# Optimization experiments

Measured on AMD Instinct MI355X. Metric: run time of the kernel, lower is better.

The kernel has to match this reference:

```python
import jax, jax.numpy as jnp
import numpy as np
from math import factorial

# ---- static configuration (matches init_kwargs) ----
IRREPS_IN1 = [(32, 0, 1), (32, 1, -1), (32, 2, 1)]   # (mul, l, parity)
IRREPS_SH  = [(1, 0, 1), (1, 1, -1), (1, 2, 1)]
IRREPS_OUT = [(32, 0, 1), (32, 1, -1), (32, 2, 1)]
NUM_BASIS = 10
HIDDEN = 16
CUTOFF = 4.0
P_ENV = 6  # dimenet envelope_exponent (5) + 1

# ---- real Wigner 3j (Clebsch-Gordan in real SH basis), computed once in numpy ----
def _su2_cg(j1, j2, j3, m1, m2, m3):
    if m3 != m1 + m2:
        return 0.0
    f = factorial
    vmin = max(-j1 + j2 + m3, -j1 + m1, 0)
    vmax = min(j2 + j3 + m1, j3 - j1 + j2, j3 + m3)
    c = (f(2*j3+1) * f(j3+j1-j2) * f(j3-j1+j2) * f(j1+j2-j3) / f(j1+j2+j3+1)
         * f(j3+m3) * f(j3-m3) / (f(j1+m1) * f(j1-m1) * f(j2+m2) * f(j2-m2))) ** 0.5
    s = 0.0
    for v in range(vmin, vmax + 1):
        s += (-1)**(v + j2 + m2) * f(j2+j3+m1-v) * f(j1-m1+v) / (
             f(v) * f(j3-j1+j2-v) * f(j3+m3-v) * f(v+j1-j2-m3))
    return c * s

def _q(l):  # real -> complex SH change of basis
    q = np.zeros((2*l+1, 2*l+1), dtype=complex)
    for m in range(-l, 0):
        q[l+m, l+abs(m)] = 2**-0.5
        q[l+m, l-abs(m)] = -1j * 2**-0.5
    q[l, l] = 1.0
    for m in range(1, l+1):
        q[l+m, l+abs(m)] = (-1)**m * 2**-0.5
        q[l+m, l-abs(m)] = 1j * (-1)**m * 2**-0.5
    return (-1j)**l * q

def _wigner_3j(l1, l2, l3):
    csu2 = np.array([[[ _su2_cg(l1, l2, l3, m1, m2, m3)
                       for m3 in range(-l3, l3+1)]
                      for m2 in range(-l2, l2+1)]
                     for m1 in range(-l1, l1+1)], dtype=complex)
    c = np.einsum('ij,kl,mn,ikm->jln', _q(l1), _q(l2), np.conj(_q(l3)), csu2)
    c = np.real(c)
    n = np.linalg.norm(c)
    return c / n if n > 0 else c

def _slices(irreps):
    s, off = [], 0
    for mul, l, p in irreps:
        d = mul * (2*l + 1)
        s.append((off, off + d))
        off += d
    return s, off

SL1, DIM_IN1 = _slices(IRREPS_IN1)
SL2, DIM_SH = _slices(IRREPS_SH)
SL3, DIM_OUT = _slices(IRREPS_OUT)

_raw = []
for i1, (m1, l1, p1) in enumerate(IRREPS_IN1):
    for i2, (m2, l2, p2) in enumerate(IRREPS_SH):
        for i3, (m3, l3, p3) in enumerate(IRREPS_OUT):
            if p1 * p2 == p3 and abs(l1 - l2) <= l3 <= l1 + l2:
                _raw.append((i1, i2, i3))

_fan = {}
for i1, i2, i3 in _raw:  # path_normalization='element': fan-in per output slot
    _fan[i3] = _fan.get(i3, 0) + IRREPS_IN1[i1][0] * IRREPS_SH[i2][0]

INSTR = []
WEIGHT_NUMEL = 0
for i1, i2, i3 in _raw:
    m1, l1, _ = IRREPS_IN1[i1]
    m2, l2, _ = IRREPS_SH[i2]
    m3, l3, _ = IRREPS_OUT[i3]
    pw = ((2*l3 + 1) / _fan[i3]) ** 0.5  # irrep_normalization='component'
    C = _wigner_3j(l1, l2, l3).astype(np.float32)
    INSTR.append((i1, i2, i3, m1, l1, m2, l2, m3, l3, WEIGHT_NUMEL, pw, C))
    WEIGHT_NUMEL += m1 * m2 * m3

# ---- radial network: Bessel basis (with dimenet envelope) -> Linear -> SiLU -> Linear ----
def _radial(distance, freq, W1, b1, W2, b2):
    d = distance[:, 0]                      # squeeze(-1) -> [E]
    x = (d / CUTOFF)[:, None]               # [E, 1]
    p = P_ENV
    a = -(p + 1) * (p + 2) / 2.0
    b = float(p * (p + 2))
    c = -p * (p + 1) / 2.0
    env = (1.0 / x + a * x**(p-1) + b * x**p + c * x**(p+1)) * (x < 1.0).astype(x.dtype)
    basis = env * jnp.sin(freq * x)         # [E, NUM_BASIS]
    h = jax.nn.silu(basis @ W1 + b1)
    return h @ W2 + b2                      # [E, WEIGHT_NUMEL]

# ---- fully connected tensor product (uvw, external per-edge weights) ----
def _tp(x, sh, weights):
    E = x.shape[0]
    acc = [jnp.zeros((E, m, 2*l + 1), x.dtype) for m, l, _ in IRREPS_OUT]
    for (i1, i2, i3, m1, l1, m2, l2, m3, l3, woff, pw, C) in INSTR:
        a, b = SL1[i1]; xb = x[:, a:b].reshape(E, m1, 2*l1 + 1)
        a, b = SL2[i2]; sb = sh[:, a:b].reshape(E, m2, 2*l2 + 1)
        w = weights[:, woff:woff + m1*m2*m3].reshape(E, m1, m2, m3)
        Cj = jnp.asarray(C)
        acc[i3] = acc[i3] + pw * jnp.einsum('euvw,ijk,eui,evj->ewk', w, Cj, xb, sb)
    return jnp.concatenate([a.reshape(E, -1) for a in acc], axis=1)


def setup_inputs() -> dict:
    key = jax.random.key(0)
    ks = jax.random.split(key, 6)
    E = 16384
    x = jax.random.normal(ks[0], (E, DIM_IN1), jnp.float32)
    rel_pos_sh = jax.random.normal(ks[1], (E, DIM_SH), jnp.float32)
    # distances strictly inside (0, cutoff) so envelope 1/x and mask are benign
    distance = 0.25 + 3.5 * jax.random.uniform(ks[2], (E, 1), jnp.float32)
    freq = jnp.pi * jnp.arange(1, NUM_BASIS + 1, dtype=jnp.float32)
    W1 = 0.4 * jax.random.normal(ks[3], (NUM_BASIS, HIDDEN), jnp.float32)
    b1 = jnp.zeros((HIDDEN,), jnp.float32)
    W2 = 0.1 * jax.random.normal(ks[4], (HIDDEN, WEIGHT_NUMEL), jnp.float32)
    b2 = jnp.zeros((WEIGHT_NUMEL,), jnp.float32)
    return {"x": x, "rel_pos_sh": rel_pos_sh, "distance": distance,
            "freq": freq, "W1": W1, "b1": b1, "W2": W2, "b2": b2}


def reference(x, rel_pos_sh, distance, freq, W1, b1, W2, b2):
    weights = _radial(distance, freq, W1, b1, W2, b2)
    return _tp(x, rel_pos_sh, weights)
```

## Files before the change

kernel.cpp:

```cpp
#include <hip/hip_runtime.h>
#include <cmath>
#include <complex>
#include <cstring>
#include <algorithm>

#define DIM_IN  288
#define DIM_SHD 9
#define NB      10
#define NH      16
#define EPB     16
#define BLOCK   256
#define NINSTR  11
#define XSTR    292
#define ZW_STRIDE 44
#define ZW_SIZE   704
#define W2B_ELEMS (NINSTR * 32 * 32 * 32)

#define OFF_XO 0
#define OFF_ZW 4672
#define OFF_SH 7488
#define POOLSZ 7680

typedef __attribute__((ext_vector_type(8))) short  short8b;
typedef __attribute__((ext_vector_type(4))) float  f32x4;
typedef __attribute__((ext_vector_type(2))) float  f32x2;

__device__ float g_C[NINSTR][125];

__device__ __forceinline__ unsigned short f2bf(float f) {
  unsigned int u = __float_as_uint(f);
  unsigned int r = (u + 0x7fffu + ((u >> 16) & 1u)) >> 16;
  return (unsigned short)r;
}

__global__ __launch_bounds__(256) void prep_w2(const float* __restrict__ W2,
                                               const float* __restrict__ b2,
                                               unsigned short* __restrict__ W2b) {
  int gid = blockIdx.x * 256 + threadIdx.x;
  if (gid < W2B_ELEMS) {
    int c = gid >> 5, t = gid & 31;
    float v = (t < 16) ? W2[(size_t)t * 11264 + c] : (t == 16 ? b2[c] : 0.0f);
    W2b[gid] = f2bf(v);
  }
}

template<int INS,int D1,int D2,int D3,int OFF1,int OFF2>
__device__ __forceinline__ void z_phase_q(
    int lane, int q, const float* __restrict__ s_x,
    const float* __restrict__ s_sh, float* __restrict__ zw)
{
  const float* __restrict__ Cp = g_C[INS];
  constexpr int NP = D3 / 2;
  #pragma unroll
  for (int s = 0; s < 2; ++s) {
    int id = lane + s * 64;
    int e = id >> 3, ul = id & 7;
    const float* xe = s_x + e * XSTR + OFF1 + (q * 8 + ul) * D1;
    f32x2 zk2[NP > 0 ? NP : 1];
    float zkl = 0.f;
    #pragma unroll
    for (int m = 0; m < NP; ++m) zk2[m] = (f32x2){0.f, 0.f};
    #pragma unroll
    for (int i = 0; i < D1; ++i) {
      float xv = xe[i];
      #pragma unroll
      for (int j = 0; j < D2; ++j) {
        float pr = xv * s_sh[e * 12 + OFF2 + j];
        f32x2 pr2 = {pr, pr};
        const float* cb = Cp + (i * D2 + j) * D3;
        #pragma unroll
        for (int m = 0; m < NP; ++m) {
          f32x2 cc = {cb[2 * m], cb[2 * m + 1]};
          zk2[m] = __builtin_elementwise_fma(cc, pr2, zk2[m]);
        }
        zkl = fmaf(cb[D3 - 1], pr, zkl);
      }
    }
    float* zo = zw + e * ZW_STRIDE + ul;
    #pragma unroll
    for (int m = 0; m < NP; ++m) {
      zo[(2 * m) * 8]     = zk2[m].x;
      zo[(2 * m + 1) * 8] = zk2[m].y;
    }
    zo[(D3 - 1) * 8] = zkl;
  }
}

template<int INS,int D3,int SB>
__device__ __forceinline__ void contract_q(
    int ls, int lq, int q,
    const unsigned short* __restrict__ W2b,
    const float* __restrict__ zw, short8b hB, f32x2 (&acc)[2][2][9])
{
  const unsigned short* Ap =
      W2b + ((size_t)(INS * 32 + q * 8) * 32 + ls) * 32 + lq * 8;
  const float* zb = zw + ls * ZW_STRIDE;
  const f32x4 zero4 = {0.f, 0.f, 0.f, 0.f};

  short8b R0c = *(const short8b*)(Ap);
  short8b R1c = *(const short8b*)(Ap + 512);
  short8b R0n = *(const short8b*)(Ap + 1024);
  short8b R1n = *(const short8b*)(Ap + 1536);
  f32x4 w0_cur = __builtin_amdgcn_mfma_f32_16x16x32_bf16(R0c, hB, zero4, 0, 0, 0);
  f32x4 w1_cur = __builtin_amdgcn_mfma_f32_16x16x32_bf16(R1c, hB, zero4, 0, 0, 0);

  #pragma unroll
  for (int c = 0; c < 2; ++c) {
    float4 zq[D3];
    #pragma unroll
    for (int k = 0; k < D3; ++k)
      zq[k] = *(const float4*)(zb + k * 8 + c * 4);
    #pragma unroll
    for (int i = 0; i < 4; ++i) {
      const int g = c * 4 + i;
      f32x4 w0n, w1n;
      if (g < 7) {
        w0n = __builtin_amdgcn_mfma_f32_16x16x32_bf16(R0n, hB, zero4, 0, 0, 0);
        w1n = __builtin_amdgcn_mfma_f32_16x16x32_bf16(R1n, hB, zero4, 0, 0, 0);
        if (g + 2 < 8) {
          R0n = *(const short8b*)(Ap + (size_t)(g + 2) * 1024);
          R1n = *(const short8b*)(Ap + (size_t)(g + 2) * 1024 + 512);
        }
      }
      f32x2 w0lo = {w0_cur[0], w0_cur[1]};
      f32x2 w0hi = {w0_cur[2], w0_cur[3]};
      f32x2 w1lo = {w1_cur[0], w1_cur[1]};
      f32x2 w1hi = {w1_cur[2], w1_cur[3]};
      #pragma unroll
      for (int k = 0; k < D3; ++k) {
        const float zz = (i == 0) ? zq[k].x : (i == 1) ? zq[k].y
                       : (i == 2) ? zq[k].z : zq[k].w;
        f32x2 zv = {zz, zz};
        acc[0][0][SB + k] = __builtin_elementwise_fma(w0lo, zv, acc[0][0][SB + k]);
        acc[0][1][SB + k] = __builtin_elementwise_fma(w0hi, zv, acc[0][1][SB + k]);
        acc[1][0][SB + k] = __builtin_elementwise_fma(w1lo, zv, acc[1][0][SB + k]);
        acc[1][1][SB + k] = __builtin_elementwise_fma(w1hi, zv, acc[1][1][SB + k]);
      }
      if (g < 7) { w0_cur = w0n; w1_cur = w1n; }
    }
  }
}

__global__ __launch_bounds__(BLOCK, 2) void conv_kernel(
    const float* __restrict__ xg, const float* __restrict__ shg,
    const float* __restrict__ dist, const float* __restrict__ freq,
    const float* __restrict__ W1, const float* __restrict__ b1,
    const unsigned short* __restrict__ W2b,
    float* __restrict__ out)
{
  __shared__ float s_pool[POOLSZ];
  float* s_xo = s_pool + OFF_XO;
  float* s_sh = s_pool + OFF_SH;

  const int tid = threadIdx.x;
  const int e0 = blockIdx.x * EPB;
  const int lane = tid & 63;
  const int ls = lane & 15;
  const int lq = lane >> 4;
  const int q   = tid >> 6;
  float* zw = s_pool + OFF_ZW + q * ZW_SIZE;
  float* s_basis = s_pool + OFF_ZW + 2 * ZW_SIZE;
  unsigned short* s_hb = (unsigned short*)(s_pool + OFF_ZW + 3 * ZW_SIZE);

  for (int i4 = tid; i4 < EPB * 72; i4 += BLOCK) {
    int e = i4 / 72, r = i4 - e * 72;
    *(float4*)(s_xo + e * XSTR + r * 4) =
        *(const float4*)(xg + (size_t)(e0 + e) * DIM_IN + r * 4);
  }
  if (tid < EPB * DIM_SHD) {
    int e = tid / DIM_SHD, c = tid - (tid / DIM_SHD) * DIM_SHD;
    s_sh[e * 12 + c] = shg[(size_t)(e0 + e) * DIM_SHD + c];
  }
  if (tid < EPB * NB) {
    int e = tid / NB, n = tid - (tid / NB) * NB;
    float d  = dist[e0 + e];
    float xv = d * 0.25f;
    float x2 = xv * xv, x4 = x2 * x2, x5 = x4 * xv;
    float env = 1.0f / xv + x5 * fmaf(xv, fmaf(xv, -21.0f, 48.0f), -28.0f);
    env = (xv < 1.0f) ? env : 0.0f;
    s_basis[e * NB + n] = env * sinf(freq[n] * xv);
  }
  __syncthreads();

  {
    int e = tid >> 4, t = tid & 15;
    float v = b1[t];
    #pragma unroll
    for (int n = 0; n < NB; ++n) v = fmaf(s_basis[e * NB + n], W1[n * NH + t], v);
    v = v / (1.0f + expf(-v));
    s_hb[e * 32 + t] = f2bf(v);
    s_hb[e * 32 + t + 16] = (t == 0) ? (unsigned short)0x3F80 : (unsigned short)0;
  }
  __syncthreads();
  short8b hB = *(const short8b*)(s_hb + ls * 32 + lq * 8);
  __syncthreads();

  f32x2 acc[2][2][9];
  #pragma unroll
  for (int wt = 0; wt < 2; ++wt)
    #pragma unroll
    for (int p = 0; p < 2; ++p)
      #pragma unroll
      for (int a = 0; a < 9; ++a) acc[wt][p][a] = (f32x2){0.f, 0.f};

  z_phase_q< 0, 1, 1, 1,   0, 0>(lane, q, s_xo, s_sh, zw);
  contract_q< 0, 1, 0>(ls, lq, q, W2b, zw, hB, acc);
  z_phase_q< 1, 1, 3, 3,   0, 1>(lane, q, s_xo, s_sh, zw);
  contract_q< 1, 3, 1>(ls, lq, q, W2b, zw, hB, acc);
  z_phase_q< 2, 1, 5, 5,   0, 4>(lane, q, s_xo, s_sh, zw);
  contract_q< 2, 5, 4>(ls, lq, q, W2b, zw, hB, acc);
  z_phase_q< 3, 3, 1, 3,  32, 0>(lane, q, s_xo, s_sh, zw);
  contract_q< 3, 3, 1>(ls, lq, q, W2b, zw, hB, acc);
  z_phase_q< 4, 3, 3, 1,  32, 1>(lane, q, s_xo, s_sh, zw);
  contract_q< 4, 1, 0>(ls, lq, q, W2b, zw, hB, acc);
  z_phase_q< 5, 3, 3, 5,  32, 1>(lane, q, s_xo, s_sh, zw);
  contract_q< 5, 5, 4>(ls, lq, q, W2b, zw, hB, acc);
  z_phase_q< 6, 3, 5, 3,  32, 4>(lane, q, s_xo, s_sh, zw);
  contract_q< 6, 3, 1>(ls, lq, q, W2b, zw, hB, acc);
  z_phase_q< 7, 5, 1, 5, 128, 0>(lane, q, s_xo, s_sh, zw);
  contract_q< 7, 5, 4>(ls, lq, q, W2b, zw, hB, acc);
  z_phase_q< 8, 5, 3, 3, 128, 1>(lane, q, s_xo, s_sh, zw);
  contract_q< 8, 3, 1>(ls, lq, q, W2b, zw, hB, acc);
  z_phase_q< 9, 5, 5, 1, 128, 4>(lane, q, s_xo, s_sh, zw);
  contract_q< 9, 1, 0>(ls, lq, q, W2b, zw, hB, acc);
  z_phase_q<10, 5, 5, 5, 128, 4>(lane, q, s_xo, s_sh, zw);
  contract_q<10, 5, 4>(ls, lq, q, W2b, zw, hB, acc);

  __syncthreads();
  #pragma unroll
  for (int ph = 3; ph >= 0; --ph) {
    if (q == ph) {
      float* row = s_xo + ls * XSTR;
      #pragma unroll
      for (int wt = 0; wt < 2; ++wt) {
        #pragma unroll
        for (int r = 0; r < 4; ++r) {
          const int w = wt * 16 + lq * 4 + r;
          float vals[9];
          #pragma unroll
          for (int a = 0; a < 9; ++a)
            vals[a] = (r & 1) ? acc[wt][r >> 1][a].y : acc[wt][r >> 1][a].x;
          if (ph == 3) {
            row[w] = vals[0];
            #pragma unroll
            for (int k = 0; k < 3; ++k) row[32 + w * 3 + k] = vals[1 + k];
            #pragma unroll
            for (int k = 0; k < 5; ++k) row[128 + w * 5 + k] = vals[4 + k];
          } else {
            row[w] += vals[0];
            #pragma unroll
            for (int k = 0; k < 3; ++k) row[32 + w * 3 + k] += vals[1 + k];
            #pragma unroll
            for (int k = 0; k < 5; ++k) row[128 + w * 5 + k] += vals[4 + k];
          }
        }
      }
    }
    __syncthreads();
  }
  for (int i4 = tid; i4 < EPB * 72; i4 += BLOCK) {
    int e = i4 / 72, r = i4 - e * 72;
    float4 v = *(const float4*)(s_xo + e * XSTR + r * 4);
    *(float4*)(out + (size_t)(e0 + e) * DIM_IN + r * 4) = v;
  }
}

typedef std::complex<double> cd;

static double factd(int n) { double r = 1; for (int i = 2; i <= n; ++i) r *= i; return r; }

static double su2_cg(int j1, int j2, int j3, int m1, int m2, int m3) {
  if (m3 != m1 + m2) return 0.0;
  int vmin = std::max(std::max(-j1 + j2 + m3, -j1 + m1), 0);
  int vmax = std::min(std::min(j2 + j3 + m1, j3 - j1 + j2), j3 + m3);
  if (vmax < vmin) return 0.0;
  double c = std::sqrt(
      factd(2*j3+1) * factd(j3+j1-j2) * factd(j3-j1+j2) * factd(j1+j2-j3) / factd(j1+j2+j3+1)
      * factd(j3+m3) * factd(j3-m3)
      / (factd(j1+m1) * factd(j1-m1) * factd(j2+m2) * factd(j2-m2)));
  double s = 0.0;
  for (int v = vmin; v <= vmax; ++v) {
    double sg = ((v + j2 + m2) & 1) ? -1.0 : 1.0;
    s += sg * factd(j2+j3+m1-v) * factd(j1-m1+v)
         / (factd(v) * factd(j3-j1+j2-v) * factd(j3+m3-v) * factd(v+j1-j2-m3));
  }
  return c * s;
}

static void qmat(int l, cd q[5][5]) {
  for (int a = 0; a < 5; ++a) for (int b = 0; b < 5; ++b) q[a][b] = cd(0, 0);
  const double s = 1.0 / std::sqrt(2.0);
  for (int m = -l; m < 0; ++m) {
    q[l + m][l - m] = cd(s, 0);
    q[l + m][l + m] = cd(0, -s);
  }
  q[l][l] = cd(1, 0);
  for (int m = 1; m <= l; ++m) {
    double sg = (m & 1) ? -1.0 : 1.0;
    q[l + m][l + m] = cd(sg * s, 0);
    q[l + m][l - m] = cd(0, sg * s);
  }
  cd ph = (l == 0) ? cd(1, 0) : (l == 1) ? cd(0, -1) : cd(-1, 0);
  for (int a = 0; a < 5; ++a) for (int b = 0; b < 5; ++b) q[a][b] *= ph;
}

static void wigner3j(int l1, int l2, int l3, double C[5][5][5]) {
  int d1 = 2*l1+1, d2 = 2*l2+1, d3 = 2*l3+1;
  cd q1[5][5], q2[5][5], q3[5][5];
  qmat(l1, q1); qmat(l2, q2); qmat(l3, q3);
  double norm2 = 0;
  for (int j = 0; j < d1; ++j)
    for (int l = 0; l < d2; ++l)
      for (int n = 0; n < d3; ++n) {
        cd sum(0, 0);
        for (int i = 0; i < d1; ++i)
          for (int k = 0; k < d2; ++k)
            for (int m = 0; m < d3; ++m) {
              double cg = su2_cg(l1, l2, l3, i - l1, k - l2, m - l3);
              if (cg != 0.0) sum += q1[i][j] * q2[k][l] * std::conj(q3[m][n]) * cg;
            }
        C[j][l][n] = sum.real();
        norm2 += C[j][l][n] * C[j][l][n];
      }
  double nrm = std::sqrt(norm2);
  if (nrm > 0)
    for (int j = 0; j < d1; ++j)
      for (int l = 0; l < d2; ++l)
        for (int n = 0; n < d3; ++n) C[j][l][n] /= nrm;
}

static void build_C_host(float C_out[NINSTR][125]) {
  const int L1[NINSTR] = {0,0,0,1,1,1,1,2,2,2,2};
  const int L2[NINSTR] = {0,1,2,0,1,1,2,0,1,2,2};
  const int L3[NINSTR] = {0,1,2,1,0,2,1,2,1,0,2};
  std::memset(C_out, 0, sizeof(float) * NINSTR * 125);
  for (int ins = 0; ins < NINSTR; ++ins) {
    int l1 = L1[ins], l2 = L2[ins], l3 = L3[ins];
    int d1 = 2*l1+1, d2 = 2*l2+1, d3 = 2*l3+1;
    double C[5][5][5];
    wigner3j(l1, l2, l3, C);
    double fan = (l3 == 0) ? 96.0 : 128.0;
    double pw = std::sqrt((2*l3+1) / fan);
    for (int i = 0; i < d1; ++i)
      for (int j = 0; j < d2; ++j)
        for (int k = 0; k < d3; ++k)
          C_out[ins][(i * d2 + j) * d3 + k] = (float)(pw * C[i][j][k]);
  }
}

extern "C" void kernel_launch(void* const* d_in, const int* in_sizes, int n_in,
                              void* d_out, int out_size, void* d_ws, size_t ws_size,
                              hipStream_t stream) {
  static float hC[NINSTR][125];
  build_C_host(hC);
  void* dC = nullptr;
  hipGetSymbolAddress(&dC, HIP_SYMBOL(g_C));
  hipMemcpyAsync(dC, hC, sizeof(hC), hipMemcpyHostToDevice, stream);

  const float* xg   = (const float*)d_in[0];
  const float* shg  = (const float*)d_in[1];
  const float* dist = (const float*)d_in[2];
  const float* freq = (const float*)d_in[3];
  const float* W1   = (const float*)d_in[4];
  const float* b1   = (const float*)d_in[5];
  const float* W2   = (const float*)d_in[6];
  const float* b2   = (const float*)d_in[7];
  float* out = (float*)d_out;
  unsigned short* W2b = (unsigned short*)d_ws;

  prep_w2<<<(W2B_ELEMS + 255) / 256, 256, 0, stream>>>(W2, b2, W2b);

  int E = in_sizes[2];
  int blocks = E / EPB;
  conv_kernel<<<blocks, BLOCK, 0, stream>>>(xg, shg, dist, freq, W1, b1, W2b, out);
}
```

Before: 70.64 us.

## Group z-phase by input irrep, load x directly from global into registers

Each wave now loads its x slice straight from global memory into registers once per input irrep and computes all of that irrep's CG-contracted z values in one pass. The results go into a larger per-wave z buffer with slot offsets, and the matching contractions then run back to back. This drops the shared-memory staging of x and repeated x reloads per instruction, and frees LDS by reusing the pool for the output gather. The cost is uncoalesced strided global loads of x, more registers held live, and a larger per-wave z buffer.

Result: faster. 68.27 us, median of 5 (-3.4%).

```diff
diff --git a/kernel.cpp b/kernel.cpp
--- a/kernel.cpp
+++ b/kernel.cpp
@@ -12,14 +12,12 @@
 #define BLOCK   256
 #define NINSTR  11
 #define XSTR    292
-#define ZW_STRIDE 44
-#define ZW_SIZE   704
+#define ZG_STRIDE 116
+#define ZG_SIZE  (16 * ZG_STRIDE)
 #define W2B_ELEMS (NINSTR * 32 * 32 * 32)
 
-#define OFF_XO 0
-#define OFF_ZW 4672
-#define OFF_SH 7488
-#define POOLSZ 7680
+#define OFF_SH 7424
+#define POOLSZ 7616
 
 typedef __attribute__((ext_vector_type(8))) short  short8b;
 typedef __attribute__((ext_vector_type(4))) float  f32x4;
@@ -44,49 +42,102 @@
   }
 }
 
-template<int INS,int D1,int D2,int D3,int OFF1,int OFF2>
-__device__ __forceinline__ void z_phase_q(
-    int lane, int q, const float* __restrict__ s_x,
-    const float* __restrict__ s_sh, float* __restrict__ zw)
+template<int INS,int D1,int D2,int D3,int OFF2,int SLOT>
+__device__ __forceinline__ void z_one(const float (&xv)[D1],
+                                      const float* __restrict__ she,
+                                      float* __restrict__ zo)
 {
   const float* __restrict__ Cp = g_C[INS];
   constexpr int NP = D3 / 2;
+  f32x2 zk2[NP > 0 ? NP : 1];
+  float zkl = 0.f;
+  #pragma unroll
+  for (int m = 0; m < NP; ++m) zk2[m] = (f32x2){0.f, 0.f};
+  #pragma unroll
+  for (int i = 0; i < D1; ++i) {
+    #pragma unroll
+    for (int j = 0; j < D2; ++j) {
+      float pr = xv[i] * she[OFF2 + j];
+      f32x2 pr2 = {pr, pr};
+      const float* cb = Cp + (i * D2 + j) * D3;
+      #pragma unroll
+      for (int m = 0; m < NP; ++m) {
+        f32x2 cc = {cb[2 * m], cb[2 * m + 1]};
+        zk2[m] = __builtin_elementwise_fma(cc, pr2, zk2[m]);
+      }
+      zkl = fmaf(cb[D3 - 1], pr, zkl);
+    }
+  }
+  #pragma unroll
+  for (int m = 0; m < NP; ++m) {
+    zo[(SLOT + 2 * m) * 8]     = zk2[m].x;
+    zo[(SLOT + 2 * m + 1) * 8] = zk2[m].y;
+  }
+  zo[(SLOT + D3 - 1) * 8] = zkl;
+}
+
+template<int D1,int OFF1>
+__device__ __forceinline__ void load_x(const float* __restrict__ xg, int e0,
+                                       int e, int u, float (&xv)[D1]) {
+  const float* xp = xg + (size_t)(e0 + e) * DIM_IN + OFF1 + u * D1;
+  #pragma unroll
+  for (int i = 0; i < D1; ++i) xv[i] = xp[i];
+}
+
+__device__ __forceinline__ void z_group_l0(int lane, int q, int e0,
+    const float* __restrict__ xg, const float* __restrict__ s_sh,
+    float* __restrict__ zw) {
   #pragma unroll
   for (int s = 0; s < 2; ++s) {
     int id = lane + s * 64;
-    int e = id >> 3, ul = id & 7;
-    const float* xe = s_x + e * XSTR + OFF1 + (q * 8 + ul) * D1;
-    f32x2 zk2[NP > 0 ? NP : 1];
-    float zkl = 0.f;
-    #pragma unroll
-    for (int m = 0; m < NP; ++m) zk2[m] = (f32x2){0.f, 0.f};
-    #pragma unroll
-    for (int i = 0; i < D1; ++i) {
-      float xv = xe[i];
-      #pragma unroll
-      for (int j = 0; j < D2; ++j) {
-        float pr = xv * s_sh[e * 12 + OFF2 + j];
-        f32x2 pr2 = {pr, pr};
-        const float* cb = Cp + (i * D2 + j) * D3;
-        #pragma unroll
-        for (int m = 0; m < NP; ++m) {
-          f32x2 cc = {cb[2 * m], cb[2 * m + 1]};
-          zk2[m] = __builtin_elementwise_fma(cc, pr2, zk2[m]);
-        }
-        zkl = fmaf(cb[D3 - 1], pr, zkl);
-      }
-    }
-    float* zo = zw + e * ZW_STRIDE + ul;
-    #pragma unroll
-    for (int m = 0; m < NP; ++m) {
-      zo[(2 * m) * 8]     = zk2[m].x;
-      zo[(2 * m + 1) * 8] = zk2[m].y;
-    }
-    zo[(D3 - 1) * 8] = zkl;
-  }
-}
-
-template<int INS,int D3,int SB>
+    int e = id >> 3, ul = id & 7, u = q * 8 + ul;
+    float xv[1];
+    load_x<1, 0>(xg, e0, e, u, xv);
+    const float* she = s_sh + e * 12;
+    float* zo = zw + e * ZG_STRIDE + ul;
+    z_one<0, 1, 1, 1, 0, 0>(xv, she, zo);
+    z_one<1, 1, 3, 3, 1, 1>(xv, she, zo);
+    z_one<2, 1, 5, 5, 4, 4>(xv, she, zo);
+  }
+}
+
+__device__ __forceinline__ void z_group_l1(int lane, int q, int e0,
+    const float* __restrict__ xg, const float* __restrict__ s_sh,
+    float* __restrict__ zw) {
+  #pragma unroll
+  for (int s = 0; s < 2; ++s) {
+    int id = lane + s * 64;
+    int e = id >> 3, ul = id & 7, u = q * 8 + ul;
+    float xv[3];
+    load_x<3, 32>(xg, e0, e, u, xv);
+    const float* she = s_sh + e * 12;
+    float* zo = zw + e * ZG_STRIDE + ul;
+    z_one<3, 3, 1, 3, 0, 0>(xv, she, zo);
+    z_one<4, 3, 3, 1, 1, 3>(xv, she, zo);
+    z_one<5, 3, 3, 5, 1, 4>(xv, she, zo);
+    z_one<6, 3, 5, 3, 4, 9>(xv, she, zo);
+  }
+}
+
+__device__ __forceinline__ void z_group_l2(int lane, int q, int e0,
+    const float* __restrict__ xg, const float* __restrict__ s_sh,
+    float* __restrict__ zw) {
+  #pragma unroll
+  for (int s = 0; s < 2; ++s) {
+    int id = lane + s * 64;
+    int e = id >> 3, ul = id & 7, u = q * 8 + ul;
+    float xv[5];
+    load_x<5, 128>(xg, e0, e, u, xv);
+    const float* she = s_sh + e * 12;
+    float* zo = zw + e * ZG_STRIDE + ul;
+    z_one< 7, 5, 1, 5, 0, 0>(xv, she, zo);
+    z_one< 8, 5, 3, 3, 1, 5>(xv, she, zo);
+    z_one< 9, 5, 5, 1, 4, 8>(xv, she, zo);
+    z_one<10, 5, 5, 5, 4, 9>(xv, she, zo);
+  }
+}
+
+template<int INS,int D3,int SB,int SLOT>
 __device__ __forceinline__ void contract_q(
     int ls, int lq, int q,
     const unsigned short* __restrict__ W2b,
@@ -94,7 +145,7 @@
 {
   const unsigned short* Ap =
       W2b + ((size_t)(INS * 32 + q * 8) * 32 + ls) * 32 + lq * 8;
-  const float* zb = zw + ls * ZW_STRIDE;
+  const float* zb = zw + ls * ZG_STRIDE + SLOT * 8;
   const f32x4 zero4 = {0.f, 0.f, 0.f, 0.f};
 
   short8b R0c = *(const short8b*)(Ap);
@@ -149,7 +200,6 @@
     float* __restrict__ out)
 {
   __shared__ float s_pool[POOLSZ];
-  float* s_xo = s_pool + OFF_XO;
   float* s_sh = s_pool + OFF_SH;
 
   const int tid = threadIdx.x;
@@ -158,15 +208,10 @@
   const int ls = lane & 15;
   const int lq = lane >> 4;
   const int q   = tid >> 6;
-  float* zw = s_pool + OFF_ZW + q * ZW_SIZE;
-  float* s_basis = s_pool + OFF_ZW + 2 * ZW_SIZE;
-  unsigned short* s_hb = (unsigned short*)(s_pool + OFF_ZW + 3 * ZW_SIZE);
-
-  for (int i4 = tid; i4 < EPB * 72; i4 += BLOCK) {
-    int e = i4 / 72, r = i4 - e * 72;
-    *(float4*)(s_xo + e * XSTR + r * 4) =
-        *(const float4*)(xg + (size_t)(e0 + e) * DIM_IN + r * 4);
-  }
+  float* zw = s_pool + q * ZG_SIZE;
+  float* s_basis = s_pool + 2 * ZG_SIZE;
+  unsigned short* s_hb = (unsigned short*)(s_pool + 3 * ZG_SIZE);
+
   if (tid < EPB * DIM_SHD) {
     int e = tid / DIM_SHD, c = tid - (tid / DIM_SHD) * DIM_SHD;
     s_sh[e * 12 + c] = shg[(size_t)(e0 + e) * DIM_SHD + c];
@@ -203,34 +248,29 @@
       #pragma unroll
       for (int a = 0; a < 9; ++a) acc[wt][p][a] = (f32x2){0.f, 0.f};
 
-  z_phase_q< 0, 1, 1, 1,   0, 0>(lane, q, s_xo, s_sh, zw);
-  contract_q< 0, 1, 0>(ls, lq, q, W2b, zw, hB, acc);
-  z_phase_q< 1, 1, 3, 3,   0, 1>(lane, q, s_xo, s_sh, zw);
-  contract_q< 1, 3, 1>(ls, lq, q, W2b, zw, hB, acc);
-  z_phase_q< 2, 1, 5, 5,   0, 4>(lane, q, s_xo, s_sh, zw);
-  contract_q< 2, 5, 4>(ls, lq, q, W2b, zw, hB, acc);
-  z_phase_q< 3, 3, 1, 3,  32, 0>(lane, q, s_xo, s_sh, zw);
-  contract_q< 3, 3, 1>(ls, lq, q, W2b, zw, hB, acc);
-  z_phase_q< 4, 3, 3, 1,  32, 1>(lane, q, s_xo, s_sh, zw);
-  contract_q< 4, 1, 0>(ls, lq, q, W2b, zw, hB, acc);
-  z_phase_q< 5, 3, 3, 5,  32, 1>(lane, q, s_xo, s_sh, zw);
-  contract_q< 5, 5, 4>(ls, lq, q, W2b, zw, hB, acc);
-  z_phase_q< 6, 3, 5, 3,  32, 4>(lane, q, s_xo, s_sh, zw);
-  contract_q< 6, 3, 1>(ls, lq, q, W2b, zw, hB, acc);
-  z_phase_q< 7, 5, 1, 5, 128, 0>(lane, q, s_xo, s_sh, zw);
-  contract_q< 7, 5, 4>(ls, lq, q, W2b, zw, hB, acc);
-  z_phase_q< 8, 5, 3, 3, 128, 1>(lane, q, s_xo, s_sh, zw);
-  contract_q< 8, 3, 1>(ls, lq, q, W2b, zw, hB, acc);
-  z_phase_q< 9, 5, 5, 1, 128, 4>(lane, q, s_xo, s_sh, zw);
-  contract_q< 9, 1, 0>(ls, lq, q, W2b, zw, hB, acc);
-  z_phase_q<10, 5, 5, 5, 128, 4>(lane, q, s_xo, s_sh, zw);
-  contract_q<10, 5, 4>(ls, lq, q, W2b, zw, hB, acc);
+  z_group_l0(lane, q, e0, xg, s_sh, zw);
+  contract_q< 0, 1, 0, 0>(ls, lq, q, W2b, zw, hB, acc);
+  contract_q< 1, 3, 1, 1>(ls, lq, q, W2b, zw, hB, acc);
+  contract_q< 2, 5, 4, 4>(ls, lq, q, W2b, zw, hB, acc);
+
+  z_group_l1(lane, q, e0, xg, s_sh, zw);
+  contract_q< 3, 3, 1, 0>(ls, lq, q, W2b, zw, hB, acc);
+  contract_q< 4, 1, 0, 3>(ls, lq, q, W2b, zw, hB, acc);
+  contract_q< 5, 5, 4, 4>(ls, lq, q, W2b, zw, hB, acc);
+  contract_q< 6, 3, 1, 9>(ls, lq, q, W2b, zw, hB, acc);
+
+  z_group_l2(lane, q, e0, xg, s_sh, zw);
+  contract_q< 7, 5, 4, 0>(ls, lq, q, W2b, zw, hB, acc);
+  contract_q< 8, 3, 1, 5>(ls, lq, q, W2b, zw, hB, acc);
+  contract_q< 9, 1, 0, 8>(ls, lq, q, W2b, zw, hB, acc);
+  contract_q<10, 5, 4, 9>(ls, lq, q, W2b, zw, hB, acc);
 
   __syncthreads();
+  float* s_og = s_pool;
   #pragma unroll
   for (int ph = 3; ph >= 0; --ph) {
     if (q == ph) {
-      float* row = s_xo + ls * XSTR;
+      float* row = s_og + ls * XSTR;
       #pragma unroll
       for (int wt = 0; wt < 2; ++wt) {
         #pragma unroll
@@ -260,7 +300,7 @@
   }
   for (int i4 = tid; i4 < EPB * 72; i4 += BLOCK) {
     int e = i4 / 72, r = i4 - e * 72;
-    float4 v = *(const float4*)(s_xo + e * XSTR + r * 4);
+    float4 v = *(const float4*)(s_og + e * XSTR + r * 4);
     *(float4*)(out + (size_t)(e0 + e) * DIM_IN + r * 4) = v;
   }
 }
```
